# Performance work log

Measured on AMD Instinct MI355X. Metric: run time of the kernel, lower is better.

The kernel has to match this reference:

```python
import jax, jax.numpy as jnp
import numpy as np

DIM_OUT = 64
ALPHA = 0.5


def setup_inputs() -> dict:
    key = jax.random.key(0)
    x = jax.random.uniform(key, (2000000, 1), dtype=jnp.float32)
    return {"x": x}


def reference(x) -> jnp.ndarray:
    # Gegenbauer polynomial recurrence, parallel over rows, sequential over order i.
    x_in = x.squeeze()                      # [n]
    c0 = jnp.ones_like(x_in)                # C_0 = 1
    c1 = 2.0 * ALPHA * x_in                 # C_1 = 2*alpha*x

    def step(carry, i):
        prev, prev2 = carry
        ci = ((2.0 * i - 2.0 + 2.0 * ALPHA) * x_in * prev
              + (-i + 2.0 - 2.0 * ALPHA) * prev2) / i
        return (ci, prev), ci

    orders = jnp.arange(2, DIM_OUT + 1, dtype=x_in.dtype)  # i = 2..dim_out
    _, cs = jax.lax.scan(step, (c1, c0), orders)           # [dim_out-1, n]
    # output is c[..., 1:] -> columns C_1..C_dim_out, shape [n, dim_out]
    out = jnp.concatenate([c1[None, :], cs], axis=0).T
    return out
```

## Files before the change

### kernel.cpp

```cpp
#include <hip/hip_runtime.h>

#define DIM_OUT 64
#define ALPHA 0.5f
#define BLOCK 256
#define NF4 (DIM_OUT / 4)

__global__ __launch_bounds__(BLOCK) void geg_kernel(const float* __restrict__ x,
                                                    float* __restrict__ out,
                                                    int n) {
    __shared__ float4 lds[BLOCK * NF4];

    const int tid = threadIdx.x;
    const size_t base_row = (size_t)blockIdx.x * BLOCK;
    const size_t row = base_row + tid;

    const float xv = (row < (size_t)n) ? x[row] : 0.0f;

    float prev2 = 1.0f;
    float prev  = 2.0f * ALPHA * xv;

    const int wsw = tid & 7;

    #pragma unroll
    for (int s = 0; s < NF4; ++s) {
        float v0, v1, v2, v3;
        #pragma unroll
        for (int k = 0; k < 4; ++k) {
            const int ord = s * 4 + k + 1;
            float ci;
            if (ord == 1) {
                ci = prev;
            } else {
                const float a   = (2.0f * (float)ord - 2.0f + 2.0f * ALPHA);
                const float b   = (-(float)ord + 2.0f - 2.0f * ALPHA);
                const float inv = 1.0f / (float)ord;
                ci = (a * xv * prev + b * prev2) * inv;
                prev2 = prev;
                prev  = ci;
            }
            if (k == 0) v0 = ci; else if (k == 1) v1 = ci;
            else if (k == 2) v2 = ci; else v3 = ci;
        }
        lds[tid * NF4 + (s ^ wsw)] = make_float4(v0, v1, v2, v3);
    }

    __syncthreads();

    #pragma unroll
    for (int j = 0; j < NF4; ++j) {
        const int f  = j * BLOCK + tid;
        const int r  = f >> 4;
        const int c4 = f & 15;
        const size_t grow = base_row + r;
        if (grow < (size_t)n) {
            float4 v = lds[r * NF4 + (c4 ^ (r & 7))];
            *(float4*)(out + grow * DIM_OUT + c4 * 4) = v;
        }
    }
}

extern "C" void kernel_launch(void* const* d_in, const int* in_sizes, int n_in,
                              void* d_out, int out_size, void* d_ws, size_t ws_size,
                              hipStream_t stream) {
    const float* x = (const float*)d_in[0];
    float* out = (float*)d_out;
    int n = in_sizes[0];

    const int grid = (n + BLOCK - 1) / BLOCK;
    geg_kernel<<<grid, BLOCK, 0, stream>>>(x, out, n);
}
```

Baseline: 503.4 us.

## Make Gegenbauer kernel persistent with grid-stride tiles and prefetched input

```diff
diff --git a/kernel.cpp b/kernel.cpp
--- a/kernel.cpp
+++ b/kernel.cpp
@@ -4,58 +4,83 @@
 #define ALPHA 0.5f
 #define BLOCK 256
 #define NF4 (DIM_OUT / 4)
+#define PERSIST_BLOCKS 512
 
 __global__ __launch_bounds__(BLOCK) void geg_kernel(const float* __restrict__ x,
                                                     float* __restrict__ out,
-                                                    int n) {
+                                                    int n, int ntiles) {
     __shared__ float4 lds[BLOCK * NF4];
 
     const int tid = threadIdx.x;
-    const size_t base_row = (size_t)blockIdx.x * BLOCK;
-    const size_t row = base_row + tid;
-
-    const float xv = (row < (size_t)n) ? x[row] : 0.0f;
-
-    float prev2 = 1.0f;
-    float prev  = 2.0f * ALPHA * xv;
-
     const int wsw = tid & 7;
 
-    #pragma unroll
-    for (int s = 0; s < NF4; ++s) {
-        float v0, v1, v2, v3;
+    int tile = blockIdx.x;
+    if (tile >= ntiles) return;
+
+    {
+        const size_t row = (size_t)tile * BLOCK + tid;
+    }
+    size_t row0 = (size_t)tile * BLOCK + tid;
+    float xv = (row0 < (size_t)n) ? x[row0] : 0.0f;
+
+    for (;;) {
+        float prev2 = 1.0f;
+        float prev  = 2.0f * ALPHA * xv;
         #pragma unroll
-        for (int k = 0; k < 4; ++k) {
-            const int ord = s * 4 + k + 1;
-            float ci;
-            if (ord == 1) {
-                ci = prev;
-            } else {
-                const float a   = (2.0f * (float)ord - 2.0f + 2.0f * ALPHA);
-                const float b   = (-(float)ord + 2.0f - 2.0f * ALPHA);
-                const float inv = 1.0f / (float)ord;
-                ci = (a * xv * prev + b * prev2) * inv;
-                prev2 = prev;
-                prev  = ci;
+        for (int s = 0; s < NF4; ++s) {
+            float v0, v1, v2, v3;
+            #pragma unroll
+            for (int k = 0; k < 4; ++k) {
+                const int ord = s * 4 + k + 1;
+                float ci;
+                if (ord == 1) {
+                    ci = prev;
+                } else {
+                    const float a   = (2.0f * (float)ord - 2.0f + 2.0f * ALPHA);
+                    const float b   = (-(float)ord + 2.0f - 2.0f * ALPHA);
+                    const float inv = 1.0f / (float)ord;
+                    ci = (a * xv * prev + b * prev2) * inv;
+                    prev2 = prev;
+                    prev  = ci;
+                }
+                if (k == 0) v0 = ci; else if (k == 1) v1 = ci;
+                else if (k == 2) v2 = ci; else v3 = ci;
             }
-            if (k == 0) v0 = ci; else if (k == 1) v1 = ci;
-            else if (k == 2) v2 = ci; else v3 = ci;
+            lds[tid * NF4 + (s ^ wsw)] = make_float4(v0, v1, v2, v3);
         }
-        lds[tid * NF4 + (s ^ wsw)] = make_float4(v0, v1, v2, v3);
-    }
 
-    __syncthreads();
+        const int next_tile = tile + (int)gridDim.x;
+        float xv_next = 0.0f;
+        if (next_tile < ntiles) {
+            const size_t nrow = (size_t)next_tile * BLOCK + tid;
+            xv_next = (nrow < (size_t)n) ? x[nrow] : 0.0f;
+        }
 
-    #pragma unroll
-    for (int j = 0; j < NF4; ++j) {
-        const int f  = j * BLOCK + tid;
-        const int r  = f >> 4;
-        const int c4 = f & 15;
-        const size_t grow = base_row + r;
-        if (grow < (size_t)n) {
-            float4 v = lds[r * NF4 + (c4 ^ (r & 7))];
-            *(float4*)(out + grow * DIM_OUT + c4 * 4) = v;
+        asm volatile("s_waitcnt lgkmcnt(0)" ::: "memory");
+        __builtin_amdgcn_s_barrier();
+        __builtin_amdgcn_sched_barrier(0);
+
+        const size_t base_row = (size_t)tile * BLOCK;
+        #pragma unroll
+        for (int j = 0; j < NF4; ++j) {
+            const int f  = j * BLOCK + tid;
+            const int r  = f >> 4;
+            const int c4 = f & 15;
+            const size_t grow = base_row + r;
+            if (grow < (size_t)n) {
+                float4 v = lds[r * NF4 + (c4 ^ (r & 7))];
+                *(float4*)(out + grow * DIM_OUT + c4 * 4) = v;
+            }
         }
+
+        if (next_tile >= ntiles) break;
+
+        asm volatile("s_waitcnt lgkmcnt(0)" ::: "memory");
+        __builtin_amdgcn_s_barrier();
+        __builtin_amdgcn_sched_barrier(0);
+
+        tile = next_tile;
+        xv = xv_next;
     }
 }
 
@@ -66,6 +91,7 @@
     float* out = (float*)d_out;
     int n = in_sizes[0];
 
-    const int grid = (n + BLOCK - 1) / BLOCK;
-    geg_kernel<<<grid, BLOCK, 0, stream>>>(x, out, n);
+    const int ntiles = (n + BLOCK - 1) / BLOCK;
+    const int grid = ntiles < PERSIST_BLOCKS ? ntiles : PERSIST_BLOCKS;
+    geg_kernel<<<grid, BLOCK, 0, stream>>>(x, out, n, ntiles);
 }
```

New measurement: 509.9 us. About the same (+1.3%).
